# Kernel optimization log

Measured on AMD Instinct MI355X. Metric: run time of the kernel, lower is better.

## Reference

```python
import jax, jax.numpy as jnp
import numpy as np

B, T, V, D, H = 64, 256, 16, 64, 256  # batch, time, n_vars, d_inp, hidden


def setup_inputs() -> dict:
    key = jax.random.key(0)
    ks = jax.random.split(key, 20)
    s = 0.02
    inp = {
        "x": jax.random.normal(ks[0], (B, T, V, D), dtype=jnp.float32),
        # weight GRN: inp = V*D, hidden = H, out = V (skip linear present since V*D != V)
        "w_fc1_w": jax.random.normal(ks[1], (V * D, H), jnp.float32) * s,
        "w_fc1_b": jnp.zeros((H,), jnp.float32),
        "w_fc2_w": jax.random.normal(ks[2], (H, V), jnp.float32) * s,
        "w_fc2_b": jnp.zeros((V,), jnp.float32),
        "w_gate_w": jax.random.normal(ks[3], (V, V), jnp.float32) * s,
        "w_gate_b": jnp.zeros((V,), jnp.float32),
        "w_skip_w": jax.random.normal(ks[4], (V * D, V), jnp.float32) * s,
        "w_skip_b": jnp.zeros((V,), jnp.float32),
        # per-variable GRNs stacked over V: inp = D, hidden = H, out = H (skip since D != H)
        "v_fc1_w": jax.random.normal(ks[5], (V, D, H), jnp.float32) * s,
        "v_fc1_b": jnp.zeros((V, H), jnp.float32),
        "v_fc2_w": jax.random.normal(ks[6], (V, H, H), jnp.float32) * s,
        "v_fc2_b": jnp.zeros((V, H), jnp.float32),
        "v_gate_w": jax.random.normal(ks[7], (V, H, H), jnp.float32) * s,
        "v_gate_b": jnp.zeros((V, H), jnp.float32),
        "v_skip_w": jax.random.normal(ks[8], (V, D, H), jnp.float32) * s,
        "v_skip_b": jnp.zeros((V, H), jnp.float32),
    }
    return inp


def reference(x, w_fc1_w, w_fc1_b, w_fc2_w, w_fc2_b, w_gate_w, w_gate_b,
              w_skip_w, w_skip_b, v_fc1_w, v_fc1_b, v_fc2_w, v_fc2_b,
              v_gate_w, v_gate_b, v_skip_w, v_skip_b):
    # dropout is identity at inference
    Bx, Tx, Vx, Dx = x.shape
    flat = x.reshape(Bx, Tx, Vx * Dx)  # [B,T,V*D]

    # --- weight GRN: (V*D) -> V ---
    h = jax.nn.elu(flat @ w_fc1_w + w_fc1_b)          # [B,T,H]
    y = h @ w_fc2_w + w_fc2_b                          # [B,T,V]
    gate = jax.nn.sigmoid(y @ w_gate_w + w_gate_b)     # [B,T,V]
    res = flat @ w_skip_w + w_skip_b                   # [B,T,V]
    w = jax.nn.softmax(res + gate * y, axis=-1)        # [B,T,V]

    # --- per-variable GRNs, batched over V: D -> H ---
    hv = jax.nn.elu(jnp.einsum('btvd,vdh->btvh', x, v_fc1_w) + v_fc1_b)        # [B,T,V,H]
    yv = jnp.einsum('btvh,vhk->btvk', hv, v_fc2_w) + v_fc2_b                   # [B,T,V,H]
    gv = jax.nn.sigmoid(jnp.einsum('btvk,vkm->btvm', yv, v_gate_w) + v_gate_b) # [B,T,V,H]
    rv = jnp.einsum('btvd,vdk->btvk', x, v_skip_w) + v_skip_b                  # [B,T,V,H]
    var_outs = rv + gv * yv                                                    # [B,T,V,H]

    # softmax-weighted sum over variables
    z = jnp.einsum('btv,btvh->bth', w, var_outs)       # [B,T,H]
    return z
```

## Files before the change

### kernel.cpp

```cpp
#include <hip/hip_runtime.h>

typedef unsigned short u16;
typedef unsigned int   u32;
typedef __bf16 bf16x8 __attribute__((ext_vector_type(8)));
typedef u16    u16x8  __attribute__((ext_vector_type(8)));
typedef float  f32x4  __attribute__((ext_vector_type(4)));

#define DI static __device__ __forceinline__

DI float b2f(u16 u){ union { u32 i; float f; } c; c.i = ((u32)u) << 16; return c.f; }
DI u16 f2b(float f){ return __builtin_bit_cast(u16, (__bf16)f); }
DI float eluf(float x){ return x > 0.f ? x : (__expf(x) - 1.f); }
DI float sigf(float x){ return 1.f / (1.f + __expf(-x)); }
DI f32x4 mfma16(bf16x8 a, bf16x8 b, f32x4 c){
  return __builtin_amdgcn_mfma_f32_16x16x32_bf16(a, b, c, 0, 0, 0);
}
DI bf16x8 ldb(const u16* p){ return *(const bf16x8*)p; }

__global__ __launch_bounds__(256) void k_pack(
    const float* __restrict__ x,
    const float* __restrict__ wfc1, const float* __restrict__ wskip,
    const float* __restrict__ vfc1, const float* __restrict__ vfc2,
    const float* __restrict__ vgate, const float* __restrict__ vskip,
    u16* __restrict__ pX, u16* __restrict__ pW1, u16* __restrict__ pF1,
    u16* __restrict__ pSk, u16* __restrict__ pF2, u16* __restrict__ pGa)
{
  __shared__ u16 sX[16 * 1032];
  const int t = threadIdx.x;
  if (blockIdx.x < 1024){
    const int rb = blockIdx.x;
    const float* xp = x + (size_t)rb * 16384;
    #pragma unroll
    for (int it = 0; it < 16; it++){
      float4 v4 = *(const float4*)&xp[it * 1024 + t * 4];
      u16 t0 = f2b(v4.x), t1 = f2b(v4.y), t2 = f2b(v4.z), t3 = f2b(v4.w);
      uint2 pk; pk.x = (u32)t0 | ((u32)t1 << 16); pk.y = (u32)t2 | ((u32)t3 << 16);
      *(uint2*)&sX[it * 1032 + t * 4] = pk;
    }
    __syncthreads();
    u16* dst = pX + (size_t)rb * 16384;
    #pragma unroll
    for (int u = 0; u < 8; u++){
      int c = u * 256 + t;
      int kc = c >> 6, lane = c & 63, ln = lane & 15, q = lane >> 4;
      u16x8 v = *(const u16x8*)&sX[ln * 1032 + kc * 32 + q * 8];
      *(uint4*)&dst[kc * 512 + lane * 8] = __builtin_bit_cast(uint4, v);
    }
    return;
  }
  const int g = (blockIdx.x - 1024) * 256 + t;
  float v8[8];
  u16* dst;
  if (g < 34816){
    int idx = g, lane = idx & 63, kc = (idx >> 6) & 31, nb = idx >> 11;
    int ln = lane & 15, q = lane >> 4;
    #pragma unroll
    for (int j = 0; j < 8; j++){
      int k = kc * 32 + q * 8 + j;
      v8[j] = (nb < 16) ? wfc1[(size_t)k * 256 + nb * 16 + ln]
                        : wskip[(size_t)k * 16 + ln];
    }
    dst = pW1 + (size_t)idx * 8;
  } else if (g < 67584){
    int idx = g - 34816, lane = idx & 63, kc = (idx >> 6) & 1, nb = (idx >> 7) & 15, v = idx >> 11;
    int ln = lane & 15, q = lane >> 4;
    #pragma unroll
    for (int j = 0; j < 8; j++){
      int k = kc * 32 + q * 8 + j;
      v8[j] = vfc1[((size_t)v * 64 + k) * 256 + nb * 16 + ln];
    }
    dst = pF1 + (size_t)idx * 8;
  } else if (g < 100352){
    int idx = g - 67584, lane = idx & 63, kc = (idx >> 6) & 1, nb = (idx >> 7) & 15, v = idx >> 11;
    int ln = lane & 15, q = lane >> 4;
    #pragma unroll
    for (int j = 0; j < 8; j++){
      int k = kc * 32 + q * 8 + j;
      v8[j] = vskip[((size_t)v * 64 + k) * 256 + nb * 16 + ln];
    }
    dst = pSk + (size_t)idx * 8;
  } else if (g < 231424){
    int idx = g - 100352, lane = idx & 63, kc = (idx >> 6) & 7, nb = (idx >> 9) & 15, v = idx >> 13;
    int ln = lane & 15, q = lane >> 4;
    #pragma unroll
    for (int j = 0; j < 8; j++){
      int k = kc * 32 + q * 8 + j;
      v8[j] = vfc2[((size_t)v * 256 + k) * 256 + nb * 16 + ln];
    }
    dst = pF2 + (size_t)idx * 8;
  } else {
    int idx = g - 231424, lane = idx & 63, kc = (idx >> 6) & 7, nb = (idx >> 9) & 15, v = idx >> 13;
    int ln = lane & 15, q = lane >> 4;
    #pragma unroll
    for (int j = 0; j < 8; j++){
      int k = kc * 32 + q * 8 + j;
      v8[j] = vgate[((size_t)v * 256 + k) * 256 + nb * 16 + ln];
    }
    dst = pGa + (size_t)idx * 8;
  }
  u16x8 tv;
  #pragma unroll
  for (int j = 0; j < 8; j++) tv[j] = f2b(v8[j]);
  *(uint4*)dst = __builtin_bit_cast(uint4, tv);
}

__global__ __launch_bounds__(512, 4) void k_fused(
    const u16* __restrict__ pX, const u16* __restrict__ pW1,
    const u16* __restrict__ pF1, const u16* __restrict__ pSk,
    const u16* __restrict__ pF2, const u16* __restrict__ pGa,
    const float* __restrict__ wb1, const float* __restrict__ W2,
    const float* __restrict__ wb2, const float* __restrict__ Wg,
    const float* __restrict__ wbg, const float* __restrict__ wbs,
    const float* __restrict__ b1, const float* __restrict__ b2,
    const float* __restrict__ bg, const float* __restrict__ bs,
    float* __restrict__ out)
{
  __shared__ __align__(16) char smem[40960];
  u16*   sHh  = (u16*)smem;
  u16*   sHy  = (u16*)(smem + 16896);
  float* sW2f = (float*)(smem + 16896);
  float* sWt  = (float*)(smem + 33792);
  float* sR   = (float*)(smem + 35840);
  float* sY   = (float*)(smem + 37888);
  float* sWgf = (float*)(smem + 39936);

  const int tid  = threadIdx.x;
  const int lane = tid & 63;
  const int wid  = tid >> 6;
  const int ln   = lane & 15;
  const int q    = lane >> 4;
  const int row0 = blockIdx.x * 32;
  const int rb0  = blockIdx.x * 2;
  const int nb0  = wid * 2;

  {
    const int ncnt = (wid == 7) ? 3 : 2;
    #pragma unroll
    for (int u = 0; u < 2; u++)
      *(float4*)&sW2f[tid * 8 + u * 4] = *(const float4*)&W2[tid * 8 + u * 4];
    if (tid < 256) sWgf[tid] = Wg[tid];

    f32x4 acc[2][3];
    #pragma unroll
    for (int mb = 0; mb < 2; mb++)
      #pragma unroll
      for (int i = 0; i < 3; i++){ acc[mb][i][0]=0.f; acc[mb][i][1]=0.f; acc[mb][i][2]=0.f; acc[mb][i][3]=0.f; }

    for (int kc = 0; kc < 32; kc++){
      bf16x8 a[2];
      #pragma unroll
      for (int mb = 0; mb < 2; mb++)
        a[mb] = ldb(&pX[((size_t)(rb0 + mb) * 32 + kc) * 512 + lane * 8]);
      #pragma unroll
      for (int i = 0; i < 3; i++){
        if (i < ncnt){
          bf16x8 b = ldb(&pW1[(size_t)((nb0 + i) * 32 + kc) * 512 + lane * 8]);
          #pragma unroll
          for (int mb = 0; mb < 2; mb++) acc[mb][i] = mfma16(a[mb], b, acc[mb][i]);
        }
      }
    }

    #pragma unroll
    for (int i = 0; i < 3; i++){
      if (i < ncnt){
        int nb = nb0 + i;
        int col = nb * 16 + ln;
        float vb = (nb < 16) ? wb1[col] : wbs[ln];
        #pragma unroll
        for (int mb = 0; mb < 2; mb++){
          #pragma unroll
          for (int r = 0; r < 4; r++){
            int lr = mb * 16 + q * 4 + r;
            float v = acc[mb][i][r] + vb;
            if (nb < 16) sHh[lr * 264 + col] = f2b(eluf(v));
            else         sR[lr * 16 + ln] = v;
          }
        }
      }
    }
    __syncthreads();

    {
      int r = tid >> 4, j = tid & 15;
      float a0 = wb2[j];
      #pragma unroll 4
      for (int kb = 0; kb < 32; kb++){
        u16x8 h8 = *(const u16x8*)&sHh[r * 264 + kb * 8];
        #pragma unroll
        for (int u = 0; u < 8; u++)
          a0 += b2f(h8[u]) * sW2f[(kb * 8 + u) * 16 + j];
      }
      sY[r * 16 + j] = a0;
    }
    __syncthreads();

    {
      int r = tid >> 4, j = tid & 15;
      float g0 = wbg[j];
      #pragma unroll
      for (int k = 0; k < 16; k++)
        g0 += sY[r * 16 + k] * sWgf[k * 16 + j];
      sWt[r * 16 + j] = sigf(g0);
    }
    __syncthreads();

    if (tid < 32){
      int r = tid;
      float l[16]; float m = -1e30f;
      #pragma unroll
      for (int j = 0; j < 16; j++){
        float v = sR[r * 16 + j] + sWt[r * 16 + j] * sY[r * 16 + j];
        l[j] = v; m = fmaxf(m, v);
      }
      float s = 0.f;
      #pragma unroll
      for (int j = 0; j < 16; j++){ l[j] = __expf(l[j] - m); s += l[j]; }
      float inv = 1.f / s;
      #pragma unroll
      for (int j = 0; j < 16; j++) sWt[r * 16 + j] = l[j] * inv;
    }
    __syncthreads();
  }

  f32x4 z[2][2];
  #pragma unroll
  for (int mb = 0; mb < 2; mb++)
    #pragma unroll
    for (int i = 0; i < 2; i++){ z[mb][i][0]=0.f; z[mb][i][1]=0.f; z[mb][i][2]=0.f; z[mb][i][3]=0.f; }

  #pragma unroll 1
  for (int v = 0; v < 16; v++){
    bf16x8 a0[2], a1[2];
    #pragma unroll
    for (int mb = 0; mb < 2; mb++){
      const u16* xp = &pX[((size_t)(rb0 + mb) * 32 + v * 2) * 512 + lane * 8];
      a0[mb] = ldb(xp);
      a1[mb] = ldb(xp + 512);
    }
    float wv[2][4];
    #pragma unroll
    for (int mb = 0; mb < 2; mb++)
      #pragma unroll
      for (int r = 0; r < 4; r++) wv[mb][r] = sWt[(mb * 16 + q * 4 + r) * 16 + v];

    f32x4 hacc[2][2];
    #pragma unroll
    for (int mb = 0; mb < 2; mb++)
      #pragma unroll
      for (int i = 0; i < 2; i++){ hacc[mb][i][0]=0.f; hacc[mb][i][1]=0.f; hacc[mb][i][2]=0.f; hacc[mb][i][3]=0.f; }
    #pragma unroll
    for (int ks = 0; ks < 2; ks++){
      bf16x8 B0 = ldb(&pF1[(size_t)((v * 16 + nb0) * 2 + ks) * 512 + lane * 8]);
      bf16x8 B1 = ldb(&pF1[(size_t)((v * 16 + nb0 + 1) * 2 + ks) * 512 + lane * 8]);
      #pragma unroll
      for (int mb = 0; mb < 2; mb++){
        bf16x8 a = ks ? a1[mb] : a0[mb];
        hacc[mb][0] = mfma16(a, B0, hacc[mb][0]);
        hacc[mb][1] = mfma16(a, B1, hacc[mb][1]);
      }
    }
    #pragma unroll
    for (int i = 0; i < 2; i++){
      int col = (nb0 + i) * 16 + ln;
      float vb = b1[v * 256 + col];
      #pragma unroll
      for (int mb = 0; mb < 2; mb++)
        #pragma unroll
        for (int r = 0; r < 4; r++)
          sHh[(mb * 16 + q * 4 + r) * 264 + col] = f2b(eluf(hacc[mb][i][r] + vb));
    }

    f32x4 racc[2][2];
    #pragma unroll
    for (int mb = 0; mb < 2; mb++)
      #pragma unroll
      for (int i = 0; i < 2; i++){ racc[mb][i][0]=0.f; racc[mb][i][1]=0.f; racc[mb][i][2]=0.f; racc[mb][i][3]=0.f; }
    #pragma unroll
    for (int ks = 0; ks < 2; ks++){
      bf16x8 B0 = ldb(&pSk[(size_t)((v * 16 + nb0) * 2 + ks) * 512 + lane * 8]);
      bf16x8 B1 = ldb(&pSk[(size_t)((v * 16 + nb0 + 1) * 2 + ks) * 512 + lane * 8]);
      #pragma unroll
      for (int mb = 0; mb < 2; mb++){
        bf16x8 a = ks ? a1[mb] : a0[mb];
        racc[mb][0] = mfma16(a, B0, racc[mb][0]);
        racc[mb][1] = mfma16(a, B1, racc[mb][1]);
      }
    }
    #pragma unroll
    for (int i = 0; i < 2; i++){
      float vb = bs[v * 256 + (nb0 + i) * 16 + ln];
      #pragma unroll
      for (int mb = 0; mb < 2; mb++)
        #pragma unroll
        for (int r = 0; r < 4; r++) z[mb][i][r] += wv[mb][r] * (racc[mb][i][r] + vb);
    }
    __syncthreads();

    f32x4 yacc[2][2];
    #pragma unroll
    for (int mb = 0; mb < 2; mb++)
      #pragma unroll
      for (int i = 0; i < 2; i++){ yacc[mb][i][0]=0.f; yacc[mb][i][1]=0.f; yacc[mb][i][2]=0.f; yacc[mb][i][3]=0.f; }
    #pragma unroll
    for (int kc = 0; kc < 8; kc++){
      bf16x8 B0 = ldb(&pF2[(size_t)((v * 16 + nb0) * 8 + kc) * 512 + lane * 8]);
      bf16x8 B1 = ldb(&pF2[(size_t)((v * 16 + nb0 + 1) * 8 + kc) * 512 + lane * 8]);
      #pragma unroll
      for (int mb = 0; mb < 2; mb++){
        bf16x8 ah = *(const bf16x8*)&sHh[(mb * 16 + ln) * 264 + kc * 32 + q * 8];
        yacc[mb][0] = mfma16(ah, B0, yacc[mb][0]);
        yacc[mb][1] = mfma16(ah, B1, yacc[mb][1]);
      }
    }
    f32x4 ysave[2][2];
    #pragma unroll
    for (int i = 0; i < 2; i++){
      int col = (nb0 + i) * 16 + ln;
      float vb = b2[v * 256 + col];
      #pragma unroll
      for (int mb = 0; mb < 2; mb++)
        #pragma unroll
        for (int r = 0; r < 4; r++){
          float yy = yacc[mb][i][r] + vb;
          ysave[mb][i][r] = yy;
          sHy[(mb * 16 + q * 4 + r) * 264 + col] = f2b(yy);
        }
    }
    __syncthreads();

    f32x4 gacc[2][2];
    #pragma unroll
    for (int mb = 0; mb < 2; mb++)
      #pragma unroll
      for (int i = 0; i < 2; i++){ gacc[mb][i][0]=0.f; gacc[mb][i][1]=0.f; gacc[mb][i][2]=0.f; gacc[mb][i][3]=0.f; }
    #pragma unroll
    for (int kc = 0; kc < 8; kc++){
      bf16x8 B0 = ldb(&pGa[(size_t)((v * 16 + nb0) * 8 + kc) * 512 + lane * 8]);
      bf16x8 B1 = ldb(&pGa[(size_t)((v * 16 + nb0 + 1) * 8 + kc) * 512 + lane * 8]);
      #pragma unroll
      for (int mb = 0; mb < 2; mb++){
        bf16x8 ah = *(const bf16x8*)&sHy[(mb * 16 + ln) * 264 + kc * 32 + q * 8];
        gacc[mb][0] = mfma16(ah, B0, gacc[mb][0]);
        gacc[mb][1] = mfma16(ah, B1, gacc[mb][1]);
      }
    }
    #pragma unroll
    for (int i = 0; i < 2; i++){
      float vb = bg[v * 256 + (nb0 + i) * 16 + ln];
      #pragma unroll
      for (int mb = 0; mb < 2; mb++)
        #pragma unroll
        for (int r = 0; r < 4; r++)
          z[mb][i][r] += wv[mb][r] * sigf(gacc[mb][i][r] + vb) * ysave[mb][i][r];
    }
  }

  #pragma unroll
  for (int i = 0; i < 2; i++){
    int col = (nb0 + i) * 16 + ln;
    #pragma unroll
    for (int mb = 0; mb < 2; mb++)
      #pragma unroll
      for (int r = 0; r < 4; r++)
        out[(size_t)(row0 + mb * 16 + q * 4 + r) * 256 + col] = z[mb][i][r];
  }
}

extern "C" void kernel_launch(void* const* d_in, const int* in_sizes, int n_in,
                              void* d_out, int out_size, void* d_ws, size_t ws_size,
                              hipStream_t stream)
{
  const float* x     = (const float*)d_in[0];
  const float* wfc1w = (const float*)d_in[1];
  const float* wfc1b = (const float*)d_in[2];
  const float* wfc2w = (const float*)d_in[3];
  const float* wfc2b = (const float*)d_in[4];
  const float* wgw   = (const float*)d_in[5];
  const float* wgb   = (const float*)d_in[6];
  const float* wsw   = (const float*)d_in[7];
  const float* wsb   = (const float*)d_in[8];
  const float* vfc1w = (const float*)d_in[9];
  const float* vfc1b = (const float*)d_in[10];
  const float* vfc2w = (const float*)d_in[11];
  const float* vfc2b = (const float*)d_in[12];
  const float* vgw   = (const float*)d_in[13];
  const float* vgb   = (const float*)d_in[14];
  const float* vsw   = (const float*)d_in[15];
  const float* vsb   = (const float*)d_in[16];

  u16* ws   = (u16*)d_ws;
  u16* pX   = ws;
  u16* pW1  = pX + 16777216;
  u16* pF1  = pW1 + 278528;
  u16* pSk  = pF1 + 262144;
  u16* pF2  = pSk + 262144;
  u16* pGa  = pF2 + 1048576;

  k_pack<<<dim3(2440), dim3(256), 0, stream>>>(
      x, wfc1w, wsw, vfc1w, vfc2w, vgw, vsw, pX, pW1, pF1, pSk, pF2, pGa);

  k_fused<<<dim3(512), dim3(512), 0, stream>>>(
      pX, pW1, pF1, pSk, pF2, pGa,
      wfc1b, wfc2w, wfc2b, wgw, wgb, wsb,
      vfc1b, vfc2b, vgb, vsb, (float*)d_out);
}
```

Measured before the change: 368.3 us.

## Software-pipeline per-variable GRN stages with double-buffered LDS, one barrier per stage

```diff
diff --git a/kernel.cpp b/kernel.cpp
--- a/kernel.cpp
+++ b/kernel.cpp
@@ -104,7 +104,141 @@
   *(uint4*)dst = __builtin_bit_cast(uint4, tv);
 }
 
-__global__ __launch_bounds__(512, 4) void k_fused(
+
+DI void fc2y(int t, int lane, int ln, int q, int nb0,
+             const u16* __restrict__ pF2, const float* __restrict__ b2,
+             const u16* h_rd, u16* y_wr, f32x4 (&ysW)[2][2])
+{
+  f32x4 yacc[2][2];
+  #pragma unroll
+  for (int mb = 0; mb < 2; mb++)
+    #pragma unroll
+    for (int i = 0; i < 2; i++){ yacc[mb][i][0]=0.f; yacc[mb][i][1]=0.f; yacc[mb][i][2]=0.f; yacc[mb][i][3]=0.f; }
+  #pragma unroll
+  for (int kc = 0; kc < 8; kc++){
+    bf16x8 B0 = ldb(&pF2[(size_t)((t * 16 + nb0) * 8 + kc) * 512 + lane * 8]);
+    bf16x8 B1 = ldb(&pF2[(size_t)((t * 16 + nb0 + 1) * 8 + kc) * 512 + lane * 8]);
+    #pragma unroll
+    for (int mb = 0; mb < 2; mb++){
+      bf16x8 ah = *(const bf16x8*)&h_rd[(mb * 16 + ln) * 264 + kc * 32 + q * 8];
+      yacc[mb][0] = mfma16(ah, B0, yacc[mb][0]);
+      yacc[mb][1] = mfma16(ah, B1, yacc[mb][1]);
+    }
+  }
+  #pragma unroll
+  for (int i = 0; i < 2; i++){
+    int col = (nb0 + i) * 16 + ln;
+    float vb = b2[t * 256 + col];
+    #pragma unroll
+    for (int mb = 0; mb < 2; mb++)
+      #pragma unroll
+      for (int r = 0; r < 4; r++){
+        float yy = yacc[mb][i][r] + vb;
+        ysW[mb][i][r * 0 + r] = yy;
+        y_wr[(mb * 16 + q * 4 + r) * 264 + col] = f2b(yy);
+      }
+  }
+}
+
+DI void gatez(int vg, int lane, int ln, int q, int nb0,
+              const u16* __restrict__ pGa, const float* __restrict__ bg,
+              const float* sWt, const u16* y_rd,
+              f32x4 (&ysR)[2][2], f32x4 (&z)[2][2])
+{
+  f32x4 gacc[2][2];
+  #pragma unroll
+  for (int mb = 0; mb < 2; mb++)
+    #pragma unroll
+    for (int i = 0; i < 2; i++){ gacc[mb][i][0]=0.f; gacc[mb][i][1]=0.f; gacc[mb][i][2]=0.f; gacc[mb][i][3]=0.f; }
+  #pragma unroll
+  for (int kc = 0; kc < 8; kc++){
+    bf16x8 B0 = ldb(&pGa[(size_t)((vg * 16 + nb0) * 8 + kc) * 512 + lane * 8]);
+    bf16x8 B1 = ldb(&pGa[(size_t)((vg * 16 + nb0 + 1) * 8 + kc) * 512 + lane * 8]);
+    #pragma unroll
+    for (int mb = 0; mb < 2; mb++){
+      bf16x8 ah = *(const bf16x8*)&y_rd[(mb * 16 + ln) * 264 + kc * 32 + q * 8];
+      gacc[mb][0] = mfma16(ah, B0, gacc[mb][0]);
+      gacc[mb][1] = mfma16(ah, B1, gacc[mb][1]);
+    }
+  }
+  float wv[2][4];
+  #pragma unroll
+  for (int mb = 0; mb < 2; mb++)
+    #pragma unroll
+    for (int r = 0; r < 4; r++) wv[mb][r] = sWt[(mb * 16 + q * 4 + r) * 16 + vg];
+  #pragma unroll
+  for (int i = 0; i < 2; i++){
+    float vb = bg[vg * 256 + (nb0 + i) * 16 + ln];
+    #pragma unroll
+    for (int mb = 0; mb < 2; mb++)
+      #pragma unroll
+      for (int r = 0; r < 4; r++)
+        z[mb][i][r] += wv[mb][r] * sigf(gacc[mb][i][r] + vb) * ysR[mb][i][r];
+  }
+}
+
+DI void fc1skip(int vn, int rb0, int lane, int ln, int q, int nb0,
+                const u16* __restrict__ pX, const u16* __restrict__ pF1,
+                const u16* __restrict__ pSk,
+                const float* __restrict__ b1, const float* __restrict__ bs,
+                const float* sWt, u16* h_wr, f32x4 (&z)[2][2])
+{
+  bf16x8 a0[2], a1[2];
+  #pragma unroll
+  for (int mb = 0; mb < 2; mb++){
+    const u16* xp = &pX[((size_t)(rb0 + mb) * 32 + vn * 2) * 512 + lane * 8];
+    a0[mb] = ldb(xp);
+    a1[mb] = ldb(xp + 512);
+  }
+  f32x4 hacc[2][2], racc[2][2];
+  #pragma unroll
+  for (int mb = 0; mb < 2; mb++)
+    #pragma unroll
+    for (int i = 0; i < 2; i++){
+      hacc[mb][i][0]=0.f; hacc[mb][i][1]=0.f; hacc[mb][i][2]=0.f; hacc[mb][i][3]=0.f;
+      racc[mb][i][0]=0.f; racc[mb][i][1]=0.f; racc[mb][i][2]=0.f; racc[mb][i][3]=0.f;
+    }
+  #pragma unroll
+  for (int ks = 0; ks < 2; ks++){
+    bf16x8 F0 = ldb(&pF1[(size_t)((vn * 16 + nb0) * 2 + ks) * 512 + lane * 8]);
+    bf16x8 F1 = ldb(&pF1[(size_t)((vn * 16 + nb0 + 1) * 2 + ks) * 512 + lane * 8]);
+    bf16x8 S0 = ldb(&pSk[(size_t)((vn * 16 + nb0) * 2 + ks) * 512 + lane * 8]);
+    bf16x8 S1 = ldb(&pSk[(size_t)((vn * 16 + nb0 + 1) * 2 + ks) * 512 + lane * 8]);
+    #pragma unroll
+    for (int mb = 0; mb < 2; mb++){
+      bf16x8 a = ks ? a1[mb] : a0[mb];
+      hacc[mb][0] = mfma16(a, F0, hacc[mb][0]);
+      hacc[mb][1] = mfma16(a, F1, hacc[mb][1]);
+      racc[mb][0] = mfma16(a, S0, racc[mb][0]);
+      racc[mb][1] = mfma16(a, S1, racc[mb][1]);
+    }
+  }
+  #pragma unroll
+  for (int i = 0; i < 2; i++){
+    int col = (nb0 + i) * 16 + ln;
+    float vb = b1[vn * 256 + col];
+    #pragma unroll
+    for (int mb = 0; mb < 2; mb++)
+      #pragma unroll
+      for (int r = 0; r < 4; r++)
+        h_wr[(mb * 16 + q * 4 + r) * 264 + col] = f2b(eluf(hacc[mb][i][r] + vb));
+  }
+  float wv[2][4];
+  #pragma unroll
+  for (int mb = 0; mb < 2; mb++)
+    #pragma unroll
+    for (int r = 0; r < 4; r++) wv[mb][r] = sWt[(mb * 16 + q * 4 + r) * 16 + vn];
+  #pragma unroll
+  for (int i = 0; i < 2; i++){
+    float vb = bs[vn * 256 + (nb0 + i) * 16 + ln];
+    #pragma unroll
+    for (int mb = 0; mb < 2; mb++)
+      #pragma unroll
+      for (int r = 0; r < 4; r++) z[mb][i][r] += wv[mb][r] * (racc[mb][i][r] + vb);
+  }
+}
+
+__global__ __launch_bounds__(512, 2) void k_fused(
     const u16* __restrict__ pX, const u16* __restrict__ pW1,
     const u16* __restrict__ pF1, const u16* __restrict__ pSk,
     const u16* __restrict__ pF2, const u16* __restrict__ pGa,
@@ -115,14 +249,16 @@
     const float* __restrict__ bg, const float* __restrict__ bs,
     float* __restrict__ out)
 {
-  __shared__ __align__(16) char smem[40960];
-  u16*   sHh  = (u16*)smem;
-  u16*   sHy  = (u16*)(smem + 16896);
-  float* sW2f = (float*)(smem + 16896);
-  float* sWt  = (float*)(smem + 33792);
-  float* sR   = (float*)(smem + 35840);
-  float* sY   = (float*)(smem + 37888);
-  float* sWgf = (float*)(smem + 39936);
+  extern __shared__ __align__(16) char smem[];
+  u16*   hb0 = (u16*)(smem);
+  u16*   hb1 = (u16*)(smem + 16896);
+  u16*   yb0 = (u16*)(smem + 33792);
+  u16*   yb1 = (u16*)(smem + 50688);
+  float* sWt = (float*)(smem + 67584);
+  float* sW2f = (float*)(smem + 33792);
+  float* sR   = (float*)(smem + 16896);
+  float* sY   = (float*)(smem + 18944);
+  float* sWgf = (float*)(smem + 20992);
 
   const int tid  = threadIdx.x;
   const int lane = tid & 63;
@@ -173,7 +309,7 @@
           for (int r = 0; r < 4; r++){
             int lr = mb * 16 + q * 4 + r;
             float v = acc[mb][i][r] + vb;
-            if (nb < 16) sHh[lr * 264 + col] = f2b(eluf(v));
+            if (nb < 16) hb0[lr * 264 + col] = f2b(eluf(v));
             else         sR[lr * 16 + ln] = v;
           }
         }
@@ -186,7 +322,7 @@
       float a0 = wb2[j];
       #pragma unroll 4
       for (int kb = 0; kb < 32; kb++){
-        u16x8 h8 = *(const u16x8*)&sHh[r * 264 + kb * 8];
+        u16x8 h8 = *(const u16x8*)&hb0[r * 264 + kb * 8];
         #pragma unroll
         for (int u = 0; u < 8; u++)
           a0 += b2f(h8[u]) * sW2f[(kb * 8 + u) * 16 + j];
@@ -223,138 +359,41 @@
     __syncthreads();
   }
 
-  f32x4 z[2][2];
-  #pragma unroll
-  for (int mb = 0; mb < 2; mb++)
-    #pragma unroll
-    for (int i = 0; i < 2; i++){ z[mb][i][0]=0.f; z[mb][i][1]=0.f; z[mb][i][2]=0.f; z[mb][i][3]=0.f; }
+  f32x4 z[2][2], ysE[2][2], ysO[2][2];
+  #pragma unroll
+  for (int mb = 0; mb < 2; mb++)
+    #pragma unroll
+    for (int i = 0; i < 2; i++){
+      z[mb][i][0]=0.f; z[mb][i][1]=0.f; z[mb][i][2]=0.f; z[mb][i][3]=0.f;
+      ysE[mb][i][0]=0.f; ysE[mb][i][1]=0.f; ysE[mb][i][2]=0.f; ysE[mb][i][3]=0.f;
+      ysO[mb][i][0]=0.f; ysO[mb][i][1]=0.f; ysO[mb][i][2]=0.f; ysO[mb][i][3]=0.f;
+    }
+
+  fc1skip(0, rb0, lane, ln, q, nb0, pX, pF1, pSk, b1, bs, sWt, hb0, z);
+  __syncthreads();
+
+  fc2y(0, lane, ln, q, nb0, pF2, b2, hb0, yb0, ysE);
+  fc1skip(1, rb0, lane, ln, q, nb0, pX, pF1, pSk, b1, bs, sWt, hb1, z);
+  __syncthreads();
 
   #pragma unroll 1
-  for (int v = 0; v < 16; v++){
-    bf16x8 a0[2], a1[2];
-    #pragma unroll
-    for (int mb = 0; mb < 2; mb++){
-      const u16* xp = &pX[((size_t)(rb0 + mb) * 32 + v * 2) * 512 + lane * 8];
-      a0[mb] = ldb(xp);
-      a1[mb] = ldb(xp + 512);
-    }
-    float wv[2][4];
-    #pragma unroll
-    for (int mb = 0; mb < 2; mb++)
-      #pragma unroll
-      for (int r = 0; r < 4; r++) wv[mb][r] = sWt[(mb * 16 + q * 4 + r) * 16 + v];
-
-    f32x4 hacc[2][2];
-    #pragma unroll
-    for (int mb = 0; mb < 2; mb++)
-      #pragma unroll
-      for (int i = 0; i < 2; i++){ hacc[mb][i][0]=0.f; hacc[mb][i][1]=0.f; hacc[mb][i][2]=0.f; hacc[mb][i][3]=0.f; }
-    #pragma unroll
-    for (int ks = 0; ks < 2; ks++){
-      bf16x8 B0 = ldb(&pF1[(size_t)((v * 16 + nb0) * 2 + ks) * 512 + lane * 8]);
-      bf16x8 B1 = ldb(&pF1[(size_t)((v * 16 + nb0 + 1) * 2 + ks) * 512 + lane * 8]);
-      #pragma unroll
-      for (int mb = 0; mb < 2; mb++){
-        bf16x8 a = ks ? a1[mb] : a0[mb];
-        hacc[mb][0] = mfma16(a, B0, hacc[mb][0]);
-        hacc[mb][1] = mfma16(a, B1, hacc[mb][1]);
-      }
-    }
-    #pragma unroll
-    for (int i = 0; i < 2; i++){
-      int col = (nb0 + i) * 16 + ln;
-      float vb = b1[v * 256 + col];
-      #pragma unroll
-      for (int mb = 0; mb < 2; mb++)
-        #pragma unroll
-        for (int r = 0; r < 4; r++)
-          sHh[(mb * 16 + q * 4 + r) * 264 + col] = f2b(eluf(hacc[mb][i][r] + vb));
-    }
-
-    f32x4 racc[2][2];
-    #pragma unroll
-    for (int mb = 0; mb < 2; mb++)
-      #pragma unroll
-      for (int i = 0; i < 2; i++){ racc[mb][i][0]=0.f; racc[mb][i][1]=0.f; racc[mb][i][2]=0.f; racc[mb][i][3]=0.f; }
-    #pragma unroll
-    for (int ks = 0; ks < 2; ks++){
-      bf16x8 B0 = ldb(&pSk[(size_t)((v * 16 + nb0) * 2 + ks) * 512 + lane * 8]);
-      bf16x8 B1 = ldb(&pSk[(size_t)((v * 16 + nb0 + 1) * 2 + ks) * 512 + lane * 8]);
-      #pragma unroll
-      for (int mb = 0; mb < 2; mb++){
-        bf16x8 a = ks ? a1[mb] : a0[mb];
-        racc[mb][0] = mfma16(a, B0, racc[mb][0]);
-        racc[mb][1] = mfma16(a, B1, racc[mb][1]);
-      }
-    }
-    #pragma unroll
-    for (int i = 0; i < 2; i++){
-      float vb = bs[v * 256 + (nb0 + i) * 16 + ln];
-      #pragma unroll
-      for (int mb = 0; mb < 2; mb++)
-        #pragma unroll
-        for (int r = 0; r < 4; r++) z[mb][i][r] += wv[mb][r] * (racc[mb][i][r] + vb);
-    }
-    __syncthreads();
-
-    f32x4 yacc[2][2];
-    #pragma unroll
-    for (int mb = 0; mb < 2; mb++)
-      #pragma unroll
-      for (int i = 0; i < 2; i++){ yacc[mb][i][0]=0.f; yacc[mb][i][1]=0.f; yacc[mb][i][2]=0.f; yacc[mb][i][3]=0.f; }
-    #pragma unroll
-    for (int kc = 0; kc < 8; kc++){
-      bf16x8 B0 = ldb(&pF2[(size_t)((v * 16 + nb0) * 8 + kc) * 512 + lane * 8]);
-      bf16x8 B1 = ldb(&pF2[(size_t)((v * 16 + nb0 + 1) * 8 + kc) * 512 + lane * 8]);
-      #pragma unroll
-      for (int mb = 0; mb < 2; mb++){
-        bf16x8 ah = *(const bf16x8*)&sHh[(mb * 16 + ln) * 264 + kc * 32 + q * 8];
-        yacc[mb][0] = mfma16(ah, B0, yacc[mb][0]);
-        yacc[mb][1] = mfma16(ah, B1, yacc[mb][1]);
-      }
-    }
-    f32x4 ysave[2][2];
-    #pragma unroll
-    for (int i = 0; i < 2; i++){
-      int col = (nb0 + i) * 16 + ln;
-      float vb = b2[v * 256 + col];
-      #pragma unroll
-      for (int mb = 0; mb < 2; mb++)
-        #pragma unroll
-        for (int r = 0; r < 4; r++){
-          float yy = yacc[mb][i][r] + vb;
-          ysave[mb][i][r] = yy;
-          sHy[(mb * 16 + q * 4 + r) * 264 + col] = f2b(yy);
-        }
-    }
-    __syncthreads();
-
-    f32x4 gacc[2][2];
-    #pragma unroll
-    for (int mb = 0; mb < 2; mb++)
-      #pragma unroll
-      for (int i = 0; i < 2; i++){ gacc[mb][i][0]=0.f; gacc[mb][i][1]=0.f; gacc[mb][i][2]=0.f; gacc[mb][i][3]=0.f; }
-    #pragma unroll
-    for (int kc = 0; kc < 8; kc++){
-      bf16x8 B0 = ldb(&pGa[(size_t)((v * 16 + nb0) * 8 + kc) * 512 + lane * 8]);
-      bf16x8 B1 = ldb(&pGa[(size_t)((v * 16 + nb0 + 1) * 8 + kc) * 512 + lane * 8]);
-      #pragma unroll
-      for (int mb = 0; mb < 2; mb++){
-        bf16x8 ah = *(const bf16x8*)&sHy[(mb * 16 + ln) * 264 + kc * 32 + q * 8];
-        gacc[mb][0] = mfma16(ah, B0, gacc[mb][0]);
-        gacc[mb][1] = mfma16(ah, B1, gacc[mb][1]);
-      }
-    }
-    #pragma unroll
-    for (int i = 0; i < 2; i++){
-      float vb = bg[v * 256 + (nb0 + i) * 16 + ln];
-      #pragma unroll
-      for (int mb = 0; mb < 2; mb++)
-        #pragma unroll
-        for (int r = 0; r < 4; r++)
-          z[mb][i][r] += wv[mb][r] * sigf(gacc[mb][i][r] + vb) * ysave[mb][i][r];
-    }
-  }
+  for (int tp = 0; tp < 7; tp++){
+    const int t = 2 * tp + 1;
+    fc2y(t, lane, ln, q, nb0, pF2, b2, hb1, yb1, ysO);
+    gatez(t - 1, lane, ln, q, nb0, pGa, bg, sWt, yb0, ysE, z);
+    fc1skip(t + 1, rb0, lane, ln, q, nb0, pX, pF1, pSk, b1, bs, sWt, hb0, z);
+    __syncthreads();
+    fc2y(t + 1, lane, ln, q, nb0, pF2, b2, hb0, yb0, ysE);
+    gatez(t, lane, ln, q, nb0, pGa, bg, sWt, yb1, ysO, z);
+    fc1skip(t + 2, rb0, lane, ln, q, nb0, pX, pF1, pSk, b1, bs, sWt, hb1, z);
+    __syncthreads();
+  }
+
+  fc2y(15, lane, ln, q, nb0, pF2, b2, hb1, yb1, ysO);
+  gatez(14, lane, ln, q, nb0, pGa, bg, sWt, yb0, ysE, z);
+  __syncthreads();
+
+  gatez(15, lane, ln, q, nb0, pGa, bg, sWt, yb1, ysO, z);
 
   #pragma unroll
   for (int i = 0; i < 2; i++){
@@ -400,7 +439,7 @@
   k_pack<<<dim3(2440), dim3(256), 0, stream>>>(
       x, wfc1w, wsw, vfc1w, vfc2w, vgw, vsw, pX, pW1, pF1, pSk, pF2, pGa);
 
-  k_fused<<<dim3(512), dim3(512), 0, stream>>>(
+  k_fused<<<dim3(512), dim3(512), 69632, stream>>>(
       pX, pW1, pF1, pSk, pF2, pGa,
       wfc1b, wfc2w, wfc2b, wgw, wgb, wsb,
       vfc1b, vfc2b, vgb, vsb, (float*)d_out);
```

Result: slower. 442.7 us (+20.2%).

## Split variable loop across two blocks, add reduce kernel, tile weight packing

Applied to the files above, without the earlier changes.

```diff
diff --git a/kernel.cpp b/kernel.cpp
--- a/kernel.cpp
+++ b/kernel.cpp
@@ -16,6 +16,27 @@
   return __builtin_amdgcn_mfma_f32_16x16x32_bf16(a, b, c, 0, 0, 0);
 }
 DI bf16x8 ldb(const u16* p){ return *(const bf16x8*)p; }
+
+DI void stage_tile(const float* __restrict__ W, int t, u16* sT){
+  #pragma unroll
+  for (int u = 0; u < 8; u++){
+    int c = u * 256 + t, row = c >> 6, colf = (c & 63) * 4;
+    float4 v4 = *(const float4*)&W[row * 256 + colf];
+    u16 a = f2b(v4.x), b = f2b(v4.y), cc = f2b(v4.z), d = f2b(v4.w);
+    uint2 pk; pk.x = (u32)a | ((u32)b << 16); pk.y = (u32)cc | ((u32)d << 16);
+    *(uint2*)&sT[row * 260 + colf] = pk;
+  }
+}
+DI void emit_tile(const u16* sT, int t, u16* dstbase, int kc, int KC){
+  #pragma unroll
+  for (int u = 0; u < 4; u++){
+    int g = u * 256 + t, nb = g >> 6, lane = g & 63, ln = lane & 15, q = lane >> 4;
+    u16x8 tv;
+    #pragma unroll
+    for (int j = 0; j < 8; j++) tv[j] = sT[(q * 8 + j) * 260 + nb * 16 + ln];
+    *(uint4*)&dstbase[((size_t)(nb * KC + kc)) * 512 + lane * 8] = __builtin_bit_cast(uint4, tv);
+  }
+}
 
 __global__ __launch_bounds__(256) void k_pack(
     const float* __restrict__ x,
@@ -48,63 +69,53 @@
     }
     return;
   }
-  const int g = (blockIdx.x - 1024) * 256 + t;
-  float v8[8];
-  u16* dst;
-  if (g < 34816){
-    int idx = g, lane = idx & 63, kc = (idx >> 6) & 31, nb = idx >> 11;
-    int ln = lane & 15, q = lane >> 4;
-    #pragma unroll
-    for (int j = 0; j < 8; j++){
-      int k = kc * 32 + q * 8 + j;
-      v8[j] = (nb < 16) ? wfc1[(size_t)k * 256 + nb * 16 + ln]
-                        : wskip[(size_t)k * 16 + ln];
-    }
-    dst = pW1 + (size_t)idx * 8;
-  } else if (g < 67584){
-    int idx = g - 34816, lane = idx & 63, kc = (idx >> 6) & 1, nb = (idx >> 7) & 15, v = idx >> 11;
-    int ln = lane & 15, q = lane >> 4;
-    #pragma unroll
-    for (int j = 0; j < 8; j++){
-      int k = kc * 32 + q * 8 + j;
-      v8[j] = vfc1[((size_t)v * 64 + k) * 256 + nb * 16 + ln];
-    }
-    dst = pF1 + (size_t)idx * 8;
-  } else if (g < 100352){
-    int idx = g - 67584, lane = idx & 63, kc = (idx >> 6) & 1, nb = (idx >> 7) & 15, v = idx >> 11;
-    int ln = lane & 15, q = lane >> 4;
-    #pragma unroll
-    for (int j = 0; j < 8; j++){
-      int k = kc * 32 + q * 8 + j;
-      v8[j] = vskip[((size_t)v * 64 + k) * 256 + nb * 16 + ln];
-    }
-    dst = pSk + (size_t)idx * 8;
-  } else if (g < 231424){
-    int idx = g - 100352, lane = idx & 63, kc = (idx >> 6) & 7, nb = (idx >> 9) & 15, v = idx >> 13;
-    int ln = lane & 15, q = lane >> 4;
-    #pragma unroll
-    for (int j = 0; j < 8; j++){
-      int k = kc * 32 + q * 8 + j;
-      v8[j] = vfc2[((size_t)v * 256 + k) * 256 + nb * 16 + ln];
-    }
-    dst = pF2 + (size_t)idx * 8;
+  const int wb = blockIdx.x - 1024;
+  if (wb == 32){
+    #pragma unroll
+    for (int u = 0; u < 64; u++){
+      int c = u * 256 + t, row = c >> 2, colf = (c & 3) * 4;
+      float4 v4 = *(const float4*)&wskip[row * 16 + colf];
+      u16 a = f2b(v4.x), b = f2b(v4.y), cc = f2b(v4.z), d = f2b(v4.w);
+      uint2 pk; pk.x = (u32)a | ((u32)b << 16); pk.y = (u32)cc | ((u32)d << 16);
+      *(uint2*)&sX[row * 16 + colf] = pk;
+    }
+    __syncthreads();
+    #pragma unroll
+    for (int u = 0; u < 8; u++){
+      int g = u * 256 + t, kc = g >> 6, lane = g & 63, ln = lane & 15, q = lane >> 4;
+      u16x8 tv;
+      #pragma unroll
+      for (int j = 0; j < 8; j++) tv[j] = sX[(kc * 32 + q * 8 + j) * 16 + ln];
+      *(uint4*)&pW1[((size_t)(16 * 32 + kc)) * 512 + lane * 8] = __builtin_bit_cast(uint4, tv);
+    }
+    return;
+  }
+  const float* src; u16* dstbase; int kc, KC;
+  if (wb < 32){
+    kc = wb; KC = 32; src = wfc1 + (size_t)kc * 32 * 256; dstbase = pW1;
+  } else if (wb < 65){
+    int idx = wb - 33, v = idx >> 1, ks = idx & 1;
+    kc = ks; KC = 2; src = vfc1 + ((size_t)v * 64 + ks * 32) * 256;
+    dstbase = pF1 + (size_t)v * 32 * 512;
+  } else if (wb < 97){
+    int idx = wb - 65, v = idx >> 1, ks = idx & 1;
+    kc = ks; KC = 2; src = vskip + ((size_t)v * 64 + ks * 32) * 256;
+    dstbase = pSk + (size_t)v * 32 * 512;
+  } else if (wb < 225){
+    int idx = wb - 97, v = idx >> 3, kk = idx & 7;
+    kc = kk; KC = 8; src = vfc2 + ((size_t)v * 256 + kk * 32) * 256;
+    dstbase = pF2 + (size_t)v * 128 * 512;
   } else {
-    int idx = g - 231424, lane = idx & 63, kc = (idx >> 6) & 7, nb = (idx >> 9) & 15, v = idx >> 13;
-    int ln = lane & 15, q = lane >> 4;
-    #pragma unroll
-    for (int j = 0; j < 8; j++){
-      int k = kc * 32 + q * 8 + j;
-      v8[j] = vgate[((size_t)v * 256 + k) * 256 + nb * 16 + ln];
-    }
-    dst = pGa + (size_t)idx * 8;
-  }
-  u16x8 tv;
-  #pragma unroll
-  for (int j = 0; j < 8; j++) tv[j] = f2b(v8[j]);
-  *(uint4*)dst = __builtin_bit_cast(uint4, tv);
-}
-
-__global__ __launch_bounds__(512, 4) void k_fused(
+    int idx = wb - 225, v = idx >> 3, kk = idx & 7;
+    kc = kk; KC = 8; src = vgate + ((size_t)v * 256 + kk * 32) * 256;
+    dstbase = pGa + (size_t)v * 128 * 512;
+  }
+  stage_tile(src, t, sX);
+  __syncthreads();
+  emit_tile(sX, t, dstbase, kc, KC);
+}
+
+__global__ __launch_bounds__(512, 8) void k_fused(
     const u16* __restrict__ pX, const u16* __restrict__ pW1,
     const u16* __restrict__ pF1, const u16* __restrict__ pSk,
     const u16* __restrict__ pF2, const u16* __restrict__ pGa,
@@ -113,32 +124,42 @@
     const float* __restrict__ wbg, const float* __restrict__ wbs,
     const float* __restrict__ b1, const float* __restrict__ b2,
     const float* __restrict__ bg, const float* __restrict__ bs,
-    float* __restrict__ out)
+    float* __restrict__ part, float* __restrict__ out)
 {
-  __shared__ __align__(16) char smem[40960];
-  u16*   sHh  = (u16*)smem;
-  u16*   sHy  = (u16*)(smem + 16896);
-  float* sW2f = (float*)(smem + 16896);
-  float* sWt  = (float*)(smem + 33792);
-  float* sR   = (float*)(smem + 35840);
-  float* sY   = (float*)(smem + 37888);
-  float* sWgf = (float*)(smem + 39936);
+  __shared__ __align__(16) char smem[35840];
+  u16*   sHh = (u16*)smem;
+  u16*   sHy = (u16*)(smem + 16896);
+  u16*   sW2 = (u16*)(smem + 16896);
+  float* sR  = (float*)(smem + 16896 + 8192);
+  float* sY  = (float*)(smem + 16896 + 10240);
+  float* sWg = (float*)(smem + 16896 + 12288);
+  float* sWt = (float*)(smem + 33792);
 
   const int tid  = threadIdx.x;
   const int lane = tid & 63;
   const int wid  = tid >> 6;
   const int ln   = lane & 15;
   const int q    = lane >> 4;
-  const int row0 = blockIdx.x * 32;
-  const int rb0  = blockIdx.x * 2;
+  const int bid  = blockIdx.x;
+  const int xcd  = bid & 7;
+  const int vhalf = xcd >> 2;
+  const int rowblk = (bid >> 3) * 4 + (bid & 3);
+  const int row0 = rowblk * 32;
+  const int rb0  = rowblk * 2;
   const int nb0  = wid * 2;
+  const int v0   = vhalf * 8;
 
   {
     const int ncnt = (wid == 7) ? 3 : 2;
-    #pragma unroll
-    for (int u = 0; u < 2; u++)
-      *(float4*)&sW2f[tid * 8 + u * 4] = *(const float4*)&W2[tid * 8 + u * 4];
-    if (tid < 256) sWgf[tid] = Wg[tid];
+    {
+      const float* wp = &W2[tid * 8];
+      float4 lo = *(const float4*)wp, hi = *(const float4*)(wp + 4);
+      u16x8 tv;
+      tv[0]=f2b(lo.x); tv[1]=f2b(lo.y); tv[2]=f2b(lo.z); tv[3]=f2b(lo.w);
+      tv[4]=f2b(hi.x); tv[5]=f2b(hi.y); tv[6]=f2b(hi.z); tv[7]=f2b(hi.w);
+      *(uint4*)&sW2[tid * 8] = __builtin_bit_cast(uint4, tv);
+      if (tid < 256) sWg[tid] = Wg[tid];
+    }
 
     f32x4 acc[2][3];
     #pragma unroll
@@ -189,7 +210,7 @@
         u16x8 h8 = *(const u16x8*)&sHh[r * 264 + kb * 8];
         #pragma unroll
         for (int u = 0; u < 8; u++)
-          a0 += b2f(h8[u]) * sW2f[(kb * 8 + u) * 16 + j];
+          a0 += b2f(h8[u]) * b2f(sW2[(kb * 8 + u) * 16 + j]);
       }
       sY[r * 16 + j] = a0;
     }
@@ -200,7 +221,7 @@
       float g0 = wbg[j];
       #pragma unroll
       for (int k = 0; k < 16; k++)
-        g0 += sY[r * 16 + k] * sWgf[k * 16 + j];
+        g0 += sY[r * 16 + k] * sWg[k * 16 + j];
       sWt[r * 16 + j] = sigf(g0);
     }
     __syncthreads();
@@ -230,7 +251,8 @@
     for (int i = 0; i < 2; i++){ z[mb][i][0]=0.f; z[mb][i][1]=0.f; z[mb][i][2]=0.f; z[mb][i][3]=0.f; }
 
   #pragma unroll 1
-  for (int v = 0; v < 16; v++){
+  for (int vi = 0; vi < 8; vi++){
+    const int v = v0 + vi;
     bf16x8 a0[2], a1[2];
     #pragma unroll
     for (int mb = 0; mb < 2; mb++){
@@ -356,6 +378,7 @@
     }
   }
 
+  float* dst = vhalf ? out : part;
   #pragma unroll
   for (int i = 0; i < 2; i++){
     int col = (nb0 + i) * 16 + ln;
@@ -363,8 +386,18 @@
     for (int mb = 0; mb < 2; mb++)
       #pragma unroll
       for (int r = 0; r < 4; r++)
-        out[(size_t)(row0 + mb * 16 + q * 4 + r) * 256 + col] = z[mb][i][r];
-  }
+        dst[(size_t)(row0 + mb * 16 + q * 4 + r) * 256 + col] = z[mb][i][r];
+  }
+}
+
+__global__ __launch_bounds__(256) void k_reduce(
+    const float* __restrict__ part, float* __restrict__ out)
+{
+  size_t i = ((size_t)blockIdx.x * 256 + threadIdx.x) * 4;
+  float4 a = *(const float4*)&part[i];
+  float4 b = *(const float4*)&out[i];
+  b.x += a.x; b.y += a.y; b.z += a.z; b.w += a.w;
+  *(float4*)&out[i] = b;
 }
 
 extern "C" void kernel_launch(void* const* d_in, const int* in_sizes, int n_in,
@@ -396,12 +429,15 @@
   u16* pSk  = pF1 + 262144;
   u16* pF2  = pSk + 262144;
   u16* pGa  = pF2 + 1048576;
-
-  k_pack<<<dim3(2440), dim3(256), 0, stream>>>(
+  float* part = (float*)(pGa + 1048576);
+
+  k_pack<<<dim3(1377), dim3(256), 0, stream>>>(
       x, wfc1w, wsw, vfc1w, vfc2w, vgw, vsw, pX, pW1, pF1, pSk, pF2, pGa);
 
-  k_fused<<<dim3(512), dim3(512), 0, stream>>>(
+  k_fused<<<dim3(1024), dim3(512), 0, stream>>>(
       pX, pW1, pF1, pSk, pF2, pGa,
       wfc1b, wfc2w, wfc2b, wgw, wgb, wsb,
-      vfc1b, vfc2b, vgb, vsb, (float*)d_out);
-}
+      vfc1b, vfc2b, vgb, vsb, part, (float*)d_out);
+
+  k_reduce<<<dim3(4096), dim3(256), 0, stream>>>(part, (float*)d_out);
+}
```

After: 655.8 us. +78.1%, slower.
